# Kernel tuning notes

Hardware: AMD Instinct MI355X
Metric: run time of the kernel (lower is better)

## Reference

```python
import jax, jax.numpy as jnp
import numpy as np

B, N, L, C, H = 8, 300, 4096, 256, 8
DH = C // H  # 32; doubled to 64 after concat with pos/sine embeddings


def _linear_params(key, fan_in, fan_out):
    kw, kb = jax.random.split(key)
    bound = 1.0 / np.sqrt(fan_in)
    W = jax.random.uniform(kw, (fan_out, fan_in), jnp.float32, -bound, bound)
    b = jax.random.uniform(kb, (fan_out,), jnp.float32, -bound, bound)
    return W, b


def setup_inputs() -> dict:
    key = jax.random.key(0)
    ks = jax.random.split(key, 13)
    inp = {
        "query": jax.random.normal(ks[0], (B, N, C), jnp.float32),
        "key": jax.random.normal(ks[1], (B, L, C), jnp.float32),
        "value": jax.random.normal(ks[2], (B, L, C), jnp.float32),
        "query_pos": jax.random.normal(ks[3], (B, N, C), jnp.float32),
        "key_pos": jax.random.normal(ks[4], (B, L, C), jnp.float32),
        "query_sine_embed": jax.random.normal(ks[5], (B, N, C), jnp.float32),
    }
    names = ["qc", "qp", "qs", "kc", "kp", "v", "o"]
    for i, nm in enumerate(names):
        W, b = _linear_params(ks[6 + i], C, C)
        inp[f"W{nm}"] = W
        inp[f"b{nm}"] = b
    return inp


def reference(query, key, value, query_pos, key_pos, query_sine_embed,
              Wqc, bqc, Wqp, bqp, Wqs, bqs, Wkc, bkc, Wkp, bkp, Wv, bv, Wo, bo):
    lin = lambda x, W, b: jnp.einsum("bnc,dc->bnd", x, W) + b
    qc = lin(query, Wqc, bqc)                  # (B, N, C)
    kc = lin(key, Wkc, bkc)                    # (B, L, C)
    v = lin(value, Wv, bv)                     # (B, L, C)
    kp = lin(key_pos, Wkp, bkp)                # (B, L, C)
    qp = lin(query_pos, Wqp, bqp)              # is_first=True branch
    q = qc + qp
    k = kc + kp
    qs = lin(query_sine_embed, Wqs, bqs)
    # split heads and concat content with positional/sine embedding -> head dim 2*DH
    q = jnp.concatenate([q.reshape(B, N, H, DH), qs.reshape(B, N, H, DH)], axis=3)   # (B,N,H,2DH)
    k = jnp.concatenate([k.reshape(B, L, H, DH), kp.reshape(B, L, H, DH)], axis=3)   # (B,L,H,2DH)
    vh = v.reshape(B, L, H, DH)
    scale = (2 * DH) ** -0.5
    attn = jnp.einsum("bnhd,blhd->bhnl", q * scale, k)      # (B,H,N,L)
    attn = jax.nn.softmax(attn, axis=-1)
    out = jnp.einsum("bhnl,blhd->bnhd", attn, vh).reshape(B, N, C)
    out = jnp.einsum("bnc,dc->bnd", out, Wo) + bo
    return query + out  # identity = query
```

## Files before the change

kernel.cpp:

```cpp
#include <hip/hip_runtime.h>
#include <hip/hip_bf16.h>

using bf8_t = __attribute__((ext_vector_type(8))) short;
using bf4_t = __attribute__((ext_vector_type(4))) short;
using u16x4 = __attribute__((ext_vector_type(4))) unsigned short;
using f32x4 = __attribute__((ext_vector_type(4))) float;

constexpr int B_   = 8;
constexpr int N_   = 300;
constexpr int L_   = 4096;
constexpr int C_   = 256;
constexpr int H_   = 8;
constexpr int NPAD = 320;
constexpr int QT_  = 5;
constexpr int SPL_ = 4;
constexpr int TPS_ = 16;
constexpr float SCALE = 0.18033688011112042f;

__device__ __forceinline__ unsigned short f2b(float f) {
  unsigned u = __float_as_uint(f);
  u += 0x7FFFu + ((u >> 16) & 1u);
  return (unsigned short)(u >> 16);
}

__device__ __forceinline__ void stage_cvt16(unsigned short* dst, const float* src) {
#pragma unroll
  for (int half = 0; half < 2; ++half) {
    f32x4 x0 = *(const f32x4*)(src + half * 8);
    f32x4 x1 = *(const f32x4*)(src + half * 8 + 4);
    bf8_t v;
#pragma unroll
    for (int j = 0; j < 4; ++j) { v[j] = (short)f2b(x0[j]); v[4 + j] = (short)f2b(x1[j]); }
    *(bf8_t*)(dst + half * 8) = v;
  }
}

__device__ __forceinline__ void gload_lds16(const void* g, void* l) {
  __builtin_amdgcn_global_load_lds(
      (const __attribute__((address_space(1))) unsigned int*)g,
      (__attribute__((address_space(3))) unsigned int*)l, 16, 0, 0);
}

__device__ __forceinline__ unsigned cvt_pk_bf16(float lo, float hi) {
  unsigned r;
  asm("v_cvt_pk_bf16_f32 %0, %1, %2" : "=v"(r) : "v"(lo), "v"(hi));
  return r;
}

__global__ __launch_bounds__(256) void wcvt_k(
    const float* __restrict__ W0, const float* __restrict__ W1, const float* __restrict__ W2,
    unsigned short* __restrict__ Wq)
{
  const float* W[3] = {W0, W1, W2};
  const int kt = blockIdx.x, i = blockIdx.y;
  const int d = threadIdx.x;
  const float* src = W[i] + (size_t)d * C_ + kt * 64;
  unsigned short* dst = Wq + ((size_t)(i * 4 + kt) * 256 + d) * 64;
#pragma unroll
  for (int g = 0; g < 8; ++g) {
    f32x4 a = *(const f32x4*)(src + g * 8);
    f32x4 b = *(const f32x4*)(src + g * 8 + 4);
    bf8_t v;
#pragma unroll
    for (int j = 0; j < 4; ++j) { v[j] = (short)f2b(a[j]); v[4 + j] = (short)f2b(b[j]); }
    *(bf8_t*)(dst + (g ^ (d & 7)) * 8) = v;
  }
}

__global__ __launch_bounds__(256) void wcvt2_k(
    const float* __restrict__ W0, const float* __restrict__ W1, const float* __restrict__ W2,
    unsigned short* __restrict__ Wk)
{
  const float* W[3] = {W0, W1, W2};
  const int kt = blockIdx.x, i = blockIdx.y;
  const int d = threadIdx.x;
  const float* src = W[i] + (size_t)d * C_ + kt * 32;
  unsigned short* dst = Wk + ((size_t)(i * 8 + kt) * 256 + d) * 32;
#pragma unroll
  for (int g = 0; g < 4; ++g) {
    f32x4 a = *(const f32x4*)(src + g * 8);
    f32x4 b = *(const f32x4*)(src + g * 8 + 4);
    bf8_t v;
#pragma unroll
    for (int j = 0; j < 4; ++j) { v[j] = (short)f2b(a[j]); v[4 + j] = (short)f2b(b[j]); }
    *(bf8_t*)(dst + (g ^ (d & 3)) * 8) = v;
  }
}

__global__ __launch_bounds__(256, 4) void kvproj_k(
    const float* __restrict__ xp, const float* __restrict__ xk, const float* __restrict__ xv,
    const unsigned short* __restrict__ Wk,
    const float* __restrict__ bkp, const float* __restrict__ bkc, const float* __restrict__ bv,
    unsigned short* __restrict__ Kc, unsigned short* __restrict__ Kp, unsigned short* __restrict__ Vt)
{
  __shared__ __align__(16) unsigned short LB[20480];
  const int tid = threadIdx.x, lane = tid & 63, wv = tid >> 6;
  const int fr = lane & 15, fg = lane >> 4;
  const int i = blockIdx.y;
  const int row0 = blockIdx.x * 64;
  const int b = row0 >> 12, ll0 = row0 & (L_ - 1);
  const float* X    = (i == 0) ? xp  : (i == 1) ? xk  : xv;
  const float* bias = (i == 0) ? bkp : (i == 1) ? bkc : bv;

  const int ar = tid >> 2, ac = tid & 3;
  const int agx = (ac ^ (ar & 3)) * 8;

  f32x4 acc[4][4] = {};

  const unsigned short* Wi = Wk + (size_t)i * 8 * 8192;

  auto stageB = [&](int step, int buf) {
    const char* src = (const char*)(Wi + step * 8192);
    char* dst = (char*)(LB + 4096 + buf * 8192);
#pragma unroll
    for (int c = 0; c < 4; ++c) {
      const int off = c * 4096 + tid * 16;
      gload_lds16(src + off, dst + off);
    }
  };
  auto stageA_load = [&](int step, f32x4* arg) {
    const float* s = X + (size_t)(row0 + ar) * C_ + step * 32 + ac * 8;
    arg[0] = *(const f32x4*)s;
    arg[1] = *(const f32x4*)(s + 4);
  };
  auto stageA_write = [&](int buf, const f32x4* arg) {
    bf8_t v;
#pragma unroll
    for (int j = 0; j < 4; ++j) { v[j] = (short)f2b(arg[0][j]); v[4 + j] = (short)f2b(arg[1][j]); }
    *(bf8_t*)(LB + buf * 2048 + ar * 32 + agx) = v;
  };

  {
    f32x4 a0[2];
    stageA_load(0, a0);
    stageB(0, 0);
    stageA_write(0, a0);
  }
  __syncthreads();

  int cur = 0;
  const int gx = (fg ^ (fr & 3)) * 8;
  for (int step = 0; step < 8; ++step) {
    const int nxt = cur ^ 1;
    f32x4 arn[2];
    if (step < 7) {
      stageA_load(step + 1, arn);
      stageB(step + 1, nxt);
    }
    const unsigned short* Ab = LB + cur * 2048;
    const unsigned short* Bb = LB + 4096 + cur * 8192;
    bf8_t xf[4];
#pragma unroll
    for (int mt = 0; mt < 4; ++mt)
      xf[mt] = *(const bf8_t*)(Ab + (mt * 16 + fr) * 32 + gx);
#pragma unroll
    for (int nt = 0; nt < 4; ++nt) {
      bf8_t wf = *(const bf8_t*)(Bb + (wv * 64 + nt * 16 + fr) * 32 + gx);
#pragma unroll
      for (int mt = 0; mt < 4; ++mt)
        acc[nt][mt] = __builtin_amdgcn_mfma_f32_16x16x32_bf16(wf, xf[mt], acc[nt][mt], 0, 0, 0);
    }
    if (step < 7) stageA_write(nxt, arn);
    __syncthreads();
    cur = nxt;
  }

  if (i < 2) {
    unsigned short* outp = (i == 0) ? Kp : Kc;
#pragma unroll
    for (int nt = 0; nt < 4; ++nt) {
      const int d0 = wv * 64 + nt * 16 + fg * 4;
      const f32x4 bb = *(const f32x4*)(bias + d0);
      const int h = d0 >> 5, dh = d0 & 31;
#pragma unroll
      for (int mt = 0; mt < 4; ++mt) {
        const int l = ll0 + mt * 16 + fr;
        u16x4 v;
#pragma unroll
        for (int r = 0; r < 4; ++r) v[r] = f2b(acc[nt][mt][r] + bb[r]);
        *(u16x4*)(outp + ((size_t)(b * H_ + h) * L_ + l) * 32 + dh) = v;
      }
    }
  } else {
    unsigned short* T = LB;
#pragma unroll
    for (int nt = 0; nt < 4; ++nt) {
      const int d0 = wv * 64 + nt * 16 + fg * 4;
      const f32x4 bb = *(const f32x4*)(bias + d0);
#pragma unroll
      for (int mt = 0; mt < 4; ++mt)
#pragma unroll
        for (int r = 0; r < 4; ++r)
          T[(d0 + r) * 68 + mt * 16 + fr] = f2b(acc[nt][mt][r] + bb[r]);
    }
    __syncthreads();
    const int d = tid;
    unsigned short* dst = Vt + ((size_t)(b * H_ + (d >> 5)) * 32 + (d & 31)) * L_ + ll0;
#pragma unroll
    for (int j = 0; j < 16; ++j)
      *(u16x4*)(dst + j * 4) = *(const u16x4*)(T + d * 68 + j * 4);
  }
}

__global__ __launch_bounds__(256, 2) void qproj_k(
    const float* __restrict__ xp, const float* __restrict__ xq, const float* __restrict__ xs,
    const unsigned short* __restrict__ Wq,
    const float* __restrict__ bqp, const float* __restrict__ bqc, const float* __restrict__ bqs,
    unsigned short* __restrict__ Qcat)
{
  __shared__ __align__(16) unsigned short Al[2][64 * 64];
  __shared__ __align__(16) unsigned short Bl[2][256 * 64];
  const int tid = threadIdx.x, lane = tid & 63, wv = tid >> 6;
  const int fr = lane & 15, fg = lane >> 4;
  const int b = blockIdx.x / 5, n0 = (blockIdx.x % 5) * 64;
  const float* Ax[3] = {xp, xq, xs};

  const int sr = tid >> 2, sc = (tid & 3) * 16;
  const int ag = sc >> 3;
  const bool arow_ok = (n0 + sr) < N_;

  f32x4 acc[16] = {};

  auto stageB = [&](int step, int buf) {
    const char* bsrc = (const char*)Wq + (size_t)step * 32768;
    char* bdst = (char*)&Bl[buf][0];
#pragma unroll
    for (int c = 0; c < 8; ++c) {
      const int off = c * 4096 + wv * 1024 + lane * 16;
      gload_lds16(bsrc + off, bdst + off);
    }
  };
  auto stageA_load = [&](int step, f32x4* ar) {
    const int i = step >> 2, kt = step & 3;
    if (arow_ok) {
      const float* src = Ax[i] + ((size_t)b * N_ + n0 + sr) * C_ + kt * 64 + sc;
#pragma unroll
      for (int j = 0; j < 4; ++j) ar[j] = *(const f32x4*)(src + j * 4);
    } else {
#pragma unroll
      for (int j = 0; j < 4; ++j) ar[j] = (f32x4){0.f, 0.f, 0.f, 0.f};
    }
  };
  auto stageA_write = [&](int buf, const f32x4* ar) {
    unsigned short* base = &Al[buf][sr * 64];
    bf8_t v0, v1;
#pragma unroll
    for (int j = 0; j < 4; ++j) {
      v0[j] = (short)f2b(ar[0][j]); v0[4 + j] = (short)f2b(ar[1][j]);
      v1[j] = (short)f2b(ar[2][j]); v1[4 + j] = (short)f2b(ar[3][j]);
    }
    *(bf8_t*)(base + ((ag ^ (sr & 7)) * 8))       = v0;
    *(bf8_t*)(base + (((ag | 1) ^ (sr & 7)) * 8)) = v1;
  };

  {
    f32x4 a0[4];
    stageA_load(0, a0);
    stageB(0, 0);
    stageA_write(0, a0);
  }
  __syncthreads();

  int cur = 0;
  const int xrow = wv * 16 + fr;
  const int n_out = n0 + wv * 16 + fr;
  const bool ok = n_out < N_;
  for (int step = 0; step < 12; ++step) {
    const int nxt = cur ^ 1;
    f32x4 arn[4];
    if (step < 11) {
      stageA_load(step + 1, arn);
      stageB(step + 1, nxt);
    }
    const unsigned short* Ab = &Al[cur][0];
    const unsigned short* Bb = &Bl[cur][0];
#pragma unroll
    for (int kh = 0; kh < 2; ++kh) {
      const int gxx = (4 * kh + fg) ^ (fr & 7);
      bf8_t xf = *(const bf8_t*)(Ab + xrow * 64 + gxx * 8);
#pragma unroll
      for (int nt = 0; nt < 16; ++nt) {
        bf8_t wf = *(const bf8_t*)(Bb + (nt * 16 + fr) * 64 + gxx * 8);
        acc[nt] = __builtin_amdgcn_mfma_f32_16x16x32_bf16(wf, xf, acc[nt], 0, 0, 0);
      }
    }
    if (step == 7 || step == 11) {
      const int off = (step == 7) ? 0 : 32;
#pragma unroll
      for (int nt = 0; nt < 16; ++nt) {
        const int d0 = nt * 16 + fg * 4;
        f32x4 bb = *(const f32x4*)(bqp + d0) + *(const f32x4*)(bqc + d0);
        if (step == 11) bb += *(const f32x4*)(bqs + d0);
        u16x4 v;
#pragma unroll
        for (int r = 0; r < 4; ++r) v[r] = ok ? f2b((acc[nt][r] + bb[r]) * SCALE) : (unsigned short)0;
        *(u16x4*)(Qcat + ((size_t)(b * H_ + (d0 >> 5)) * NPAD + n_out) * 64 + off + (d0 & 31)) = v;
      }
    }
    if (step < 11) stageA_write(nxt, arn);
    __syncthreads();
    cur = nxt;
  }
}

__global__ __launch_bounds__(256, 5) void attn_k(
    const unsigned short* __restrict__ Qcat, const unsigned short* __restrict__ Kc,
    const unsigned short* __restrict__ Kp, const unsigned short* __restrict__ Vt,
    float* __restrict__ PO, float* __restrict__ PM, float* __restrict__ PLs)
{
  __shared__ __align__(16) unsigned short Kcl[2][64 * 32];
  __shared__ __align__(16) unsigned short Kpl[2][64 * 32];
  __shared__ __align__(16) unsigned short Vp[2][32][72];
  const int x = blockIdx.x;
  const int qt = x >> 8;
  const int rem = x & 255;
  const int s = rem & (SPL_ - 1);
  const int h = (rem >> 2) & (H_ - 1);
  const int b = rem >> 5;
  const int n0 = qt * 64;
  const int tid = threadIdx.x, lane = tid & 63, wv = tid >> 6;
  const int fr = lane & 15, fg = lane >> 4;

  const unsigned short* Qb = Qcat + ((size_t)b * H_ + h) * NPAD * 64;
  bf8_t qf[2];
  {
    const int qrow = n0 + wv * 16 + fr;
    qf[0] = *(const bf8_t*)&Qb[(size_t)qrow * 64 + 8 * fg];
    qf[1] = *(const bf8_t*)&Qb[(size_t)qrow * 64 + 32 + 8 * fg];
  }
  float m_r = -1e30f, l_r = 0.f;
  f32x4 o[2] = {};

  const unsigned short* KcB = Kc + ((size_t)b * H_ + h) * L_ * 32;
  const unsigned short* KpB = Kp + ((size_t)b * H_ + h) * L_ * 32;
  const unsigned short* VB  = Vt + ((size_t)b * H_ + h) * 32 * (size_t)L_;

  const int koff = tid * 16;
  const int vd = tid >> 3, vc = (tid & 7) * 8;

  auto stageK = [&](int t, int buf) {
    gload_lds16((const char*)KcB + (size_t)t * 4096 + koff, (char*)&Kcl[buf][0] + koff);
    gload_lds16((const char*)KpB + (size_t)t * 4096 + koff, (char*)&Kpl[buf][0] + koff);
  };

  const int t0 = s * TPS_, t1 = t0 + TPS_;

  stageK(t0, 0);
  bf8_t vreg = *(const bf8_t*)(VB + (size_t)vd * L_ + t0 * 64 + vc);

  int cur = 0;
  for (int t = t0; t < t1; ++t) {
    *(bf8_t*)&Vp[cur][vd][vc] = vreg;
    __syncthreads();
    if (t + 1 < t1) {
      stageK(t + 1, cur ^ 1);
      vreg = *(const bf8_t*)(VB + (size_t)vd * L_ + (t + 1) * 64 + vc);
    }
    f32x4 sc[4] = {};
#pragma unroll
    for (int nf = 0; nf < 4; ++nf) {
      const int kro = (nf * 16 + fr) * 32 + 8 * fg;
      bf8_t kf0 = *(const bf8_t*)&Kcl[cur][kro];
      bf8_t kf1 = *(const bf8_t*)&Kpl[cur][kro];
      sc[nf] = __builtin_amdgcn_mfma_f32_16x16x32_bf16(kf0, qf[0], sc[nf], 0, 0, 0);
      sc[nf] = __builtin_amdgcn_mfma_f32_16x16x32_bf16(kf1, qf[1], sc[nf], 0, 0, 0);
    }
    float mx = fmaxf(fmaxf(sc[0][0], sc[0][1]), fmaxf(sc[0][2], sc[0][3]));
#pragma unroll
    for (int nf = 1; nf < 4; ++nf)
      mx = fmaxf(mx, fmaxf(fmaxf(sc[nf][0], sc[nf][1]), fmaxf(sc[nf][2], sc[nf][3])));
    mx = fmaxf(mx, __shfl_xor(mx, 16));
    mx = fmaxf(mx, __shfl_xor(mx, 32));
    const float mnew = fmaxf(m_r, mx);
    const float corr = exp2f(m_r - mnew);
    float ps = 0.f;
#pragma unroll
    for (int nf = 0; nf < 4; ++nf)
#pragma unroll
      for (int r = 0; r < 4; ++r) {
        const float p = exp2f(sc[nf][r] - mnew);
        sc[nf][r] = p;
        ps += p;
      }
    ps += __shfl_xor(ps, 16);
    ps += __shfl_xor(ps, 32);
    l_r = l_r * corr + ps;
    m_r = mnew;
#pragma unroll
    for (int r = 0; r < 4; ++r) { o[0][r] *= corr; o[1][r] *= corr; }
    unsigned pw[8];
#pragma unroll
    for (int nf = 0; nf < 4; ++nf) {
      pw[2 * nf]     = cvt_pk_bf16(sc[nf][0], sc[nf][1]);
      pw[2 * nf + 1] = cvt_pk_bf16(sc[nf][2], sc[nf][3]);
    }
#pragma unroll
    for (int kh = 0; kh < 2; ++kh) {
      union { unsigned u[4]; bf8_t v; } pu;
      pu.u[0] = pw[4 * kh];     pu.u[1] = pw[4 * kh + 1];
      pu.u[2] = pw[4 * kh + 2]; pu.u[3] = pw[4 * kh + 3];
      const bf8_t pf = pu.v;
#pragma unroll
      for (int df = 0; df < 2; ++df) {
        const unsigned short* vrow = &Vp[cur][df * 16 + fr][0];
        bf4_t va = *(const bf4_t*)(vrow + kh * 32 + fg * 4);
        bf4_t vb = *(const bf4_t*)(vrow + kh * 32 + 16 + fg * 4);
        bf8_t vf;
#pragma unroll
        for (int j = 0; j < 4; ++j) { vf[j] = va[j]; vf[4 + j] = vb[j]; }
        o[df] = __builtin_amdgcn_mfma_f32_16x16x32_bf16(vf, pf, o[df], 0, 0, 0);
      }
    }
    cur ^= 1;
  }
  const int rec = (((b * H_) + h) * QT_ + qt) * SPL_ + s;
  const int q = wv * 16 + fr;
  if (fg == 0) {
    PM [rec * 64 + q] = m_r;
    PLs[rec * 64 + q] = l_r;
  }
#pragma unroll
  for (int df = 0; df < 2; ++df)
    *(f32x4*)(PO + ((size_t)rec * 64 + q) * 32 + df * 16 + fg * 4) = o[df];
}

__global__ __launch_bounds__(256) void combine_k(
    const float* __restrict__ PO, const float* __restrict__ PM, const float* __restrict__ PLs,
    unsigned short* __restrict__ aout)
{
  const int qt = blockIdx.x, h = blockIdx.y, b = blockIdx.z;
  const int tid = threadIdx.x;
  const int row = tid >> 2, dh0 = (tid & 3) * 8;
  const int rec0 = (((b * H_) + h) * QT_ + qt) * SPL_;
  float m[SPL_], w[SPL_];
  float M = -1e30f;
#pragma unroll
  for (int s = 0; s < SPL_; ++s) { m[s] = PM[(rec0 + s) * 64 + row]; M = fmaxf(M, m[s]); }
  float denom = 0.f;
#pragma unroll
  for (int s = 0; s < SPL_; ++s) {
    w[s] = exp2f(m[s] - M);
    denom += w[s] * PLs[(rec0 + s) * 64 + row];
  }
  float num[8] = {};
#pragma unroll
  for (int s = 0; s < SPL_; ++s) {
    const float* po = PO + ((size_t)(rec0 + s) * 64 + row) * 32 + dh0;
    f32x4 a = *(const f32x4*)po;
    f32x4 c = *(const f32x4*)(po + 4);
#pragma unroll
    for (int j = 0; j < 4; ++j) { num[j] += w[s] * a[j]; num[4 + j] += w[s] * c[j]; }
  }
  const int n = qt * 64 + row;
  if (n < N_) {
    const float inv = 1.f / denom;
    bf8_t v;
#pragma unroll
    for (int j = 0; j < 8; ++j) v[j] = (short)f2b(num[j] * inv);
    *(bf8_t*)(aout + ((size_t)b * NPAD + n) * C_ + h * 32 + dh0) = v;
  }
}

__global__ __launch_bounds__(256) void oproj_k(
    const unsigned short* __restrict__ aout, const float* __restrict__ Wo,
    const float* __restrict__ bo, const float* __restrict__ query,
    float* __restrict__ out)
{
  __shared__ __align__(16) unsigned short Al[64][72];
  __shared__ __align__(16) unsigned short Bl[64][72];
  const int b = blockIdx.z, n0 = blockIdx.y * 64, d0 = blockIdx.x * 64;
  const int tid = threadIdx.x, lane = tid & 63, wv = tid >> 6;
  const int wm = wv >> 1, wn = wv & 1;
  const int sr = tid >> 2, sc = (tid & 3) * 16;
  const int fr = lane & 15, fg = lane >> 4;
  f32x4 acc[2][2] = {};

  for (int kt = 0; kt < 4; ++kt) {
    const int k0 = kt * 64;
    {
      const unsigned short* src = aout + ((size_t)b * NPAD + n0 + sr) * C_ + k0 + sc;
      *(bf8_t*)&Al[sr][sc]     = *(const bf8_t*)src;
      *(bf8_t*)&Al[sr][sc + 8] = *(const bf8_t*)(src + 8);
    }
    stage_cvt16(&Bl[sr][sc], Wo + (size_t)(d0 + sr) * C_ + k0 + sc);
    __syncthreads();
#pragma unroll
    for (int kh = 0; kh < 2; ++kh) {
      const int ko = kh * 32 + 8 * fg;
      bf8_t af[2], bq[2];
#pragma unroll
      for (int m = 0; m < 2; ++m) {
        af[m] = *(const bf8_t*)&Al[wm * 32 + m * 16 + fr][ko];
        bq[m] = *(const bf8_t*)&Bl[wn * 32 + m * 16 + fr][ko];
      }
#pragma unroll
      for (int m = 0; m < 2; ++m)
#pragma unroll
        for (int n = 0; n < 2; ++n)
          acc[m][n] = __builtin_amdgcn_mfma_f32_16x16x32_bf16(af[m], bq[n], acc[m][n], 0, 0, 0);
    }
    __syncthreads();
  }
#pragma unroll
  for (int m = 0; m < 2; ++m)
#pragma unroll
    for (int nn = 0; nn < 2; ++nn) {
      const int d = d0 + wn * 32 + nn * 16 + fr;
      const float bb = bo[d];
#pragma unroll
      for (int r = 0; r < 4; ++r) {
        const int n = n0 + wm * 32 + m * 16 + fg * 4 + r;
        if (n < N_) {
          const size_t gi = ((size_t)b * N_ + n) * C_ + d;
          out[gi] = acc[m][nn][r] + bb + query[gi];
        }
      }
    }
}

extern "C" void kernel_launch(void* const* d_in, const int* in_sizes, int n_in,
                              void* d_out, int out_size, void* d_ws, size_t ws_size,
                              hipStream_t stream)
{
  const float* query = (const float*)d_in[0];
  const float* key   = (const float*)d_in[1];
  const float* value = (const float*)d_in[2];
  const float* qpos  = (const float*)d_in[3];
  const float* kpos  = (const float*)d_in[4];
  const float* qsine = (const float*)d_in[5];
  const float* Wqc = (const float*)d_in[6];  const float* bqc = (const float*)d_in[7];
  const float* Wqp = (const float*)d_in[8];  const float* bqp = (const float*)d_in[9];
  const float* Wqs = (const float*)d_in[10]; const float* bqs = (const float*)d_in[11];
  const float* Wkc = (const float*)d_in[12]; const float* bkc = (const float*)d_in[13];
  const float* Wkp = (const float*)d_in[14]; const float* bkp = (const float*)d_in[15];
  const float* Wv  = (const float*)d_in[16]; const float* bv  = (const float*)d_in[17];
  const float* Wo  = (const float*)d_in[18]; const float* bo  = (const float*)d_in[19];

  const size_t qcat_b = (size_t)B_ * H_ * NPAD * 64 * 2;
  const size_t kc_b   = (size_t)B_ * H_ * L_ * 32 * 2;
  const size_t kp_b   = kc_b;
  const size_t vt_b   = kc_b;
  const size_t aout_b = (size_t)B_ * NPAD * C_ * 2;
  const size_t nrec   = (size_t)B_ * H_ * QT_ * SPL_;
  const size_t po_b   = nrec * 64 * 32 * 4;
  const size_t pm_b   = nrec * 64 * 4;
  const size_t pl_b   = nrec * 64 * 4;
  const size_t wsw_b  = (size_t)24 * 256 * 64 * 2;
  if (ws_size < qcat_b + kc_b + kp_b + vt_b + aout_b + po_b + pm_b + pl_b + wsw_b) return;
  char* ws = (char*)d_ws;
  unsigned short* Qcat = (unsigned short*)(ws);
  unsigned short* Kc   = (unsigned short*)(ws + qcat_b);
  unsigned short* Kp   = (unsigned short*)(ws + qcat_b + kc_b);
  unsigned short* Vt   = (unsigned short*)(ws + qcat_b + kc_b + kp_b);
  unsigned short* aout = (unsigned short*)(ws + qcat_b + kc_b + kp_b + vt_b);
  float* PO  = (float*)(ws + qcat_b + kc_b + kp_b + vt_b + aout_b);
  float* PM  = (float*)(ws + qcat_b + kc_b + kp_b + vt_b + aout_b + po_b);
  float* PLs = (float*)(ws + qcat_b + kc_b + kp_b + vt_b + aout_b + po_b + pm_b);
  unsigned short* Wq = (unsigned short*)(ws + qcat_b + kc_b + kp_b + vt_b + aout_b + po_b + pm_b + pl_b);
  unsigned short* Wk = Wq + (size_t)12 * 16384;
  float* out = (float*)d_out;

  wcvt_k   <<<dim3(4, 3),                 256, 0, stream>>>(Wqp, Wqc, Wqs, Wq);
  wcvt2_k  <<<dim3(8, 3),                 256, 0, stream>>>(Wkp, Wkc, Wv, Wk);
  qproj_k  <<<dim3(B_ * QT_),             256, 0, stream>>>(qpos, query, qsine, Wq, bqp, bqc, bqs, Qcat);
  kvproj_k <<<dim3(512, 3),               256, 0, stream>>>(kpos, key, value, Wk, bkp, bkc, bv, Kc, Kp, Vt);
  attn_k   <<<dim3(QT_ * SPL_ * B_ * H_), 256, 0, stream>>>(Qcat, Kc, Kp, Vt, PO, PM, PLs);
  combine_k<<<dim3(QT_, 8, 8),            256, 0, stream>>>(PO, PM, PLs, aout);
  oproj_k  <<<dim3(4, QT_, 8),            256, 0, stream>>>(aout, Wo, bo, query, out);
}
```

Baseline: 131.4 us.

## Pad K tiles in LDS via register staging and skip online-softmax rescale lazily

Replaces direct global-to-LDS loads of the K content/position tiles with register loads that are then written into a padded LDS layout (row stride 36 elements), so MFMA fragment reads avoid bank conflicts. It also adds a lazy online-softmax rescale: the running max and the accumulator correction are updated only when some lane's new max exceeds the stored max by more than 8 (in log2 units). The register staging adds VGPR pressure and split 8-byte LDS accesses. The lazy rescale lets exponentials go up to 2^8 before correction, which is safe for fp32 accumulation.

```diff
diff --git a/kernel.cpp b/kernel.cpp
--- a/kernel.cpp
+++ b/kernel.cpp
@@ -308,8 +308,8 @@
     const unsigned short* __restrict__ Kp, const unsigned short* __restrict__ Vt,
     float* __restrict__ PO, float* __restrict__ PM, float* __restrict__ PLs)
 {
-  __shared__ __align__(16) unsigned short Kcl[2][64 * 32];
-  __shared__ __align__(16) unsigned short Kpl[2][64 * 32];
+  __shared__ __align__(16) unsigned short Kcl[2][64 * 36];
+  __shared__ __align__(16) unsigned short Kpl[2][64 * 36];
   __shared__ __align__(16) unsigned short Vp[2][32][72];
   const int x = blockIdx.x;
   const int qt = x >> 8;
@@ -335,33 +335,52 @@
   const unsigned short* KpB = Kp + ((size_t)b * H_ + h) * L_ * 32;
   const unsigned short* VB  = Vt + ((size_t)b * H_ + h) * 32 * (size_t)L_;
 
-  const int koff = tid * 16;
+  const int sl = tid >> 2, sg = tid & 3;
   const int vd = tid >> 3, vc = (tid & 7) * 8;
 
-  auto stageK = [&](int t, int buf) {
-    gload_lds16((const char*)KcB + (size_t)t * 4096 + koff, (char*)&Kcl[buf][0] + koff);
-    gload_lds16((const char*)KpB + (size_t)t * 4096 + koff, (char*)&Kpl[buf][0] + koff);
+  auto loadK = [&](int t, bf8_t* kc2, bf8_t* kp2) {
+    const size_t off = ((size_t)(t * 64 + sl)) * 32 + sg * 8;
+    *kc2 = *(const bf8_t*)(KcB + off);
+    *kp2 = *(const bf8_t*)(KpB + off);
   };
 
   const int t0 = s * TPS_, t1 = t0 + TPS_;
-
-  stageK(t0, 0);
-  bf8_t vreg = *(const bf8_t*)(VB + (size_t)vd * L_ + t0 * 64 + vc);
+  bf8_t kcr, kpr, vreg;
+  loadK(t0, &kcr, &kpr);
+  vreg = *(const bf8_t*)(VB + (size_t)vd * L_ + t0 * 64 + vc);
 
   int cur = 0;
   for (int t = t0; t < t1; ++t) {
-    *(bf8_t*)&Vp[cur][vd][vc] = vreg;
+    {
+      unsigned short* kd = &Kcl[cur][sl * 36 + sg * 8];
+      unsigned short* pd = &Kpl[cur][sl * 36 + sg * 8];
+      bf4_t lo, hi;
+#pragma unroll
+      for (int j = 0; j < 4; ++j) { lo[j] = kcr[j]; hi[j] = kcr[4 + j]; }
+      *(bf4_t*)kd = lo; *(bf4_t*)(kd + 4) = hi;
+#pragma unroll
+      for (int j = 0; j < 4; ++j) { lo[j] = kpr[j]; hi[j] = kpr[4 + j]; }
+      *(bf4_t*)pd = lo; *(bf4_t*)(pd + 4) = hi;
+      *(bf8_t*)&Vp[cur][vd][vc] = vreg;
+    }
     __syncthreads();
     if (t + 1 < t1) {
-      stageK(t + 1, cur ^ 1);
+      loadK(t + 1, &kcr, &kpr);
       vreg = *(const bf8_t*)(VB + (size_t)vd * L_ + (t + 1) * 64 + vc);
     }
     f32x4 sc[4] = {};
 #pragma unroll
     for (int nf = 0; nf < 4; ++nf) {
-      const int kro = (nf * 16 + fr) * 32 + 8 * fg;
-      bf8_t kf0 = *(const bf8_t*)&Kcl[cur][kro];
-      bf8_t kf1 = *(const bf8_t*)&Kpl[cur][kro];
+      const unsigned short* pc = &Kcl[cur][(nf * 16 + fr) * 36 + 8 * fg];
+      const unsigned short* pp = &Kpl[cur][(nf * 16 + fr) * 36 + 8 * fg];
+      bf4_t c0 = *(const bf4_t*)pc, c1 = *(const bf4_t*)(pc + 4);
+      bf4_t p0 = *(const bf4_t*)pp, p1 = *(const bf4_t*)(pp + 4);
+      bf8_t kf0, kf1;
+#pragma unroll
+      for (int j = 0; j < 4; ++j) {
+        kf0[j] = c0[j]; kf0[4 + j] = c1[j];
+        kf1[j] = p0[j]; kf1[4 + j] = p1[j];
+      }
       sc[nf] = __builtin_amdgcn_mfma_f32_16x16x32_bf16(kf0, qf[0], sc[nf], 0, 0, 0);
       sc[nf] = __builtin_amdgcn_mfma_f32_16x16x32_bf16(kf1, qf[1], sc[nf], 0, 0, 0);
     }
@@ -371,23 +390,26 @@
       mx = fmaxf(mx, fmaxf(fmaxf(sc[nf][0], sc[nf][1]), fmaxf(sc[nf][2], sc[nf][3])));
     mx = fmaxf(mx, __shfl_xor(mx, 16));
     mx = fmaxf(mx, __shfl_xor(mx, 32));
-    const float mnew = fmaxf(m_r, mx);
-    const float corr = exp2f(m_r - mnew);
+    if (!__all(mx <= m_r + 8.f)) {
+      const float mnew = fmaxf(m_r, mx);
+      const float corr = exp2f(m_r - mnew);
+      l_r *= corr;
+#pragma unroll
+      for (int r = 0; r < 4; ++r) { o[0][r] *= corr; o[1][r] *= corr; }
+      m_r = mnew;
+    }
     float ps = 0.f;
 #pragma unroll
     for (int nf = 0; nf < 4; ++nf)
 #pragma unroll
       for (int r = 0; r < 4; ++r) {
-        const float p = exp2f(sc[nf][r] - mnew);
+        const float p = exp2f(sc[nf][r] - m_r);
         sc[nf][r] = p;
         ps += p;
       }
     ps += __shfl_xor(ps, 16);
     ps += __shfl_xor(ps, 32);
-    l_r = l_r * corr + ps;
-    m_r = mnew;
-#pragma unroll
-    for (int r = 0; r < 4; ++r) { o[0][r] *= corr; o[1][r] *= corr; }
+    l_r += ps;
     unsigned pw[8];
 #pragma unroll
     for (int nf = 0; nf < 4; ++nf) {
```

After: 128.2 us. 2.4% less time.
